# Optimization experiments

Measured on AMD Instinct MI355X. Metric: run time of the kernel, lower is better.

## Reference

```python
import jax, jax.numpy as jnp
import numpy as np

NS = (128, 128, 128)       # ns_mesh
NODES = 4                  # interpolation_nodes (P3M, even -> floor-based indexing)
N_POINTS = 100000
N_CHANNELS = 8
BOX = 10.0


def _weights_p3m4(x):
    # x: (P, 3) relative offsets in [-1/2, 1/2]; returns (4, P, 3)
    x2 = x * x
    x3 = x * x2
    c = jnp.asarray(1.0 / 48.0, dtype=x.dtype)
    return jnp.stack([
        c * (1 - 6 * x + 12 * x2 - 8 * x3),
        c * (23 - 30 * x - 12 * x2 + 24 * x3),
        c * (23 + 30 * x - 12 * x2 - 24 * x3),
        c * (1 + 6 * x + 12 * x2 + 8 * x3),
    ])


def setup_inputs() -> dict:
    key = jax.random.key(0)
    k1, k2 = jax.random.split(key)
    positions = jax.random.uniform(k1, (N_POINTS, 3), dtype=jnp.float32) * BOX
    particle_weights = jax.random.normal(k2, (N_POINTS, N_CHANNELS), dtype=jnp.float32)
    cell = jnp.eye(3, dtype=jnp.float32) * BOX
    return {"positions": positions, "particle_weights": particle_weights, "cell": cell}


def reference(positions, particle_weights, cell):
    nx, ny, nz = NS
    ns_f = jnp.array(NS, dtype=positions.dtype)
    inv_cell = jnp.linalg.inv(cell)

    # --- compute_weights ---
    pos_rel = ns_f * (positions @ inv_cell)        # (P,3) mesh-scaled fractional coords
    idx0 = jnp.floor(pos_rel)                      # even nodes -> floor of position
    offsets = pos_rel - (idx0 + 0.5)               # in [-1/2, 1/2]
    w = _weights_p3m4(offsets)                     # (4, P, 3) per-axis 1d weights
    shifts = jnp.arange(1 - (NODES + 1) // 2, 1 + NODES // 2, dtype=jnp.int32)  # [-1,0,1,2]
    ns_i = jnp.array(NS, dtype=jnp.int32)
    idx = (idx0.astype(jnp.int32)[None] + shifts[:, None, None]) % ns_i  # (4,P,3) periodic
    xi, yi, zi = idx[..., 0], idx[..., 1], idx[..., 2]  # (4,P) each

    # 3D outer product of per-axis weights: (4,4,4,P)
    w3 = w[:, None, None, :, 0] * w[None, :, None, :, 1] * w[None, None, :, :, 2]
    # flattened mesh index per (i,j,k,point): (4,4,4,P)
    lin = (xi[:, None, None] * ny + yi[None, :, None]) * nz + zi[None, None, :]

    # --- points_to_mesh: scatter-add weighted charges onto mesh ---
    C = particle_weights.shape[1]
    vals = w3[..., None] * particle_weights        # (4,4,4,P,C)
    rho_flat = jnp.zeros((nx * ny * nz, C), dtype=positions.dtype)
    rho_flat = rho_flat.at[lin.reshape(-1)].add(vals.reshape(-1, C))

    # --- mesh_to_points: gather mesh values back to particle positions ---
    gathered = rho_flat[lin]                       # (4,4,4,P,C)
    out = jnp.sum(gathered * w3[..., None], axis=(0, 1, 2))  # (P,C)
    return out
```

## Files before the change

kernel.cpp:

```cpp
#include <hip/hip_runtime.h>

static constexpr int NXC   = 128;
static constexpr int NPTS  = 100000;
static constexpr int NCH   = 8;
static constexpr int TS    = 8;
static constexpr int NT    = 16;
static constexpr int NTILES = NT * NT * NT;
static constexpr int SLOT  = 64;
static constexpr int REC   = 20;
static constexpr int SLABCAP = 32;
static constexpr int AMAX  = 14 * SLABCAP;
static constexpr int NMAX  = 48;
static constexpr int NGRP  = 32;

__device__ __forceinline__ void axis_weights(float x, float w[4]) {
    float x2 = x * x, x3 = x2 * x;
    const float c = 1.0f / 48.0f;
    w[0] = c * (1.0f  - 6.0f  * x + 12.0f * x2 - 8.0f  * x3);
    w[1] = c * (23.0f - 30.0f * x - 12.0f * x2 + 24.0f * x3);
    w[2] = c * (23.0f + 30.0f * x - 12.0f * x2 - 24.0f * x3);
    w[3] = c * (1.0f  + 6.0f  * x + 12.0f * x2 + 8.0f  * x3);
}

__device__ __forceinline__ void mesh_coords(const float* __restrict__ pos,
                                            const float* __restrict__ cell,
                                            int p, float& rx, float& ry, float& rz) {
    float a = cell[0], b = cell[1], c = cell[2];
    float d = cell[3], e = cell[4], f = cell[5];
    float g = cell[6], h = cell[7], i9 = cell[8];
    float c00 = e * i9 - f * h, c01 = f * g - d * i9, c02 = d * h - e * g;
    float c10 = c * h - b * i9, c11 = a * i9 - c * g, c12 = b * g - a * h;
    float c20 = b * f - c * e,  c21 = c * d - a * f,  c22 = a * e - b * d;
    float det = a * c00 + b * c01 + c * c02;
    float s = 128.0f / det;
    float p0 = pos[p * 3 + 0], p1 = pos[p * 3 + 1], p2 = pos[p * 3 + 2];
    rx = s * (p0 * c00 + p1 * c01 + p2 * c02);
    ry = s * (p0 * c10 + p1 * c11 + p2 * c12);
    rz = s * (p0 * c20 + p1 * c21 + p2 * c22);
}

__global__ __launch_bounds__(256) void bin_k(const float* __restrict__ pos,
                                             const float* __restrict__ pw,
                                             const float* __restrict__ cell,
                                             int* __restrict__ cursor,
                                             int* __restrict__ scell,
                                             int* __restrict__ spid,
                                             float* __restrict__ srec) {
    int p = blockIdx.x * 256 + threadIdx.x;
    if (p >= NPTS) return;
    float rx, ry, rz;
    mesh_coords(pos, cell, p, rx, ry, rz);
    float fx = floorf(rx), fy = floorf(ry), fz = floorf(rz);
    int ix = ((int)fx) & (NXC - 1), iy = ((int)fy) & (NXC - 1), iz = ((int)fz) & (NXC - 1);
    int tile = ((ix >> 3) * NT + (iy >> 3)) * NT + (iz >> 3);
    int slot = atomicAdd(cursor + tile, 1);
    if (slot >= SLOT) return;
    int idx = tile * SLOT + slot;
    scell[idx] = ix | (iy << 10) | (iz << 20);
    spid[idx] = p;
    float wx[4], wy[4], wz[4];
    axis_weights(rx - fx - 0.5f, wx);
    axis_weights(ry - fy - 0.5f, wy);
    axis_weights(rz - fz - 0.5f, wz);
    float4* r = reinterpret_cast<float4*>(srec) + (size_t)idx * 5;
    r[0] = make_float4(wx[0], wx[1], wx[2], wx[3]);
    r[1] = make_float4(wy[0], wy[1], wy[2], wy[3]);
    r[2] = make_float4(wz[0], wz[1], wz[2], wz[3]);
    const float4* pw4 = reinterpret_cast<const float4*>(pw + (size_t)p * NCH);
    r[3] = pw4[0];
    r[4] = pw4[1];
}

__device__ __forceinline__ float corr4(float4 wp, float4 wq, int d) {
    float s0 = d == 0 ? wq.x : d == -1 ? wq.y : d == -2 ? wq.z : d == -3 ? wq.w : 0.0f;
    float s1 = d == 1 ? wq.x : d ==  0 ? wq.y : d == -1 ? wq.z : d == -2 ? wq.w : 0.0f;
    float s2 = d == 2 ? wq.x : d ==  1 ? wq.y : d ==  0 ? wq.z : d == -1 ? wq.w : 0.0f;
    float s3 = d == 3 ? wq.x : d ==  2 ? wq.y : d ==  1 ? wq.z : d ==  0 ? wq.w : 0.0f;
    return wp.x * s0 + wp.y * s1 + wp.z * s2 + wp.w * s3;
}

__global__ __launch_bounds__(256) void pair_k(const int* __restrict__ cursor,
                                              const int* __restrict__ scell,
                                              const int* __restrict__ spid,
                                              const float* __restrict__ srec,
                                              float* __restrict__ out) {
    __shared__ int2 slab[AMAX];
    __shared__ int2 A12[AMAX];
    __shared__ int nlist[NGRP * NMAX];
    __shared__ int scnt[14];
    __shared__ int soff[15];

    int b = blockIdx.x;
    int tx = b >> 8, ty = (b >> 4) & 15, tz = b & 15;
    int tid = threadIdx.x;
    int lane = tid & 63;
    int nown = min(cursor[b], SLOT);
    if (nown == 0) return;
    int begin = b * SLOT;

    if (tid < 14) scnt[tid] = 0;
    __syncthreads();

    int crew = tid >> 3, cl = tid & 7;
    int base_x = tx * TS - 3, base_y = ty * TS - 3, base_z = tz * TS - 3;
    if (crew < 27) {
        int ox = crew / 9 - 1, oy = (crew / 3) % 3 - 1, oz = crew % 3 - 1;
        int nt = ((((tx + ox) & 15) * NT + ((ty + oy) & 15)) * NT) + ((tz + oz) & 15);
        int n0 = nt * SLOT;
        int cn = min(cursor[nt], SLOT);
        for (int s0 = 0; s0 < cn; s0 += 8) {
            int s = s0 + cl;
            if (s < cn) {
                int i = n0 + s;
                int c = scell[i];
                int lcx = ((c & 1023) - base_x) & 127;
                int lcy = (((c >> 10) & 1023) - base_y) & 127;
                int lcz = (((c >> 20) & 1023) - base_z) & 127;
                if (lcx < 14 && lcy < 14 && lcz < 14) {
                    int slot = atomicAdd(&scnt[lcx], 1);
                    if (slot < SLABCAP)
                        slab[lcx * SLABCAP + slot] =
                            make_int2(lcy | (lcz << 5) | (lcx << 10), i);
                }
            }
        }
    }
    __syncthreads();
    if (tid == 0) {
        int run = 0;
        #pragma unroll
        for (int s2 = 0; s2 < 14; ++s2) {
            soff[s2] = run;
            run += min(scnt[s2], SLABCAP);
        }
        soff[14] = run;
    }
    __syncthreads();
    for (int u = tid; u < AMAX; u += 256) {
        int s2 = u >> 5, i2 = u & (SLABCAP - 1);
        if (i2 < min(scnt[s2], SLABCAP)) A12[soff[s2] + i2] = slab[u];
    }
    __syncthreads();

    int sub = tid & 7, pg = tid >> 3;
    const float4* recs = reinterpret_cast<const float4*>(srec);
    int nbl = pg * NMAX;

    for (int p = pg; __any(p < nown); p += NGRP) {
        bool live = p < nown;
        int lpx = 0, lpyh = 0, lpzh = 0, jbeg = 0, span = 0, pid = 0;
        float4 pxw, pyw, pzw;
        if (live) {
            int pc = scell[begin + p];
            lpx  = (pc & 1023) - tx * TS;
            lpyh = ((pc >> 10) & 1023) - ty * TS + 3;
            lpzh = ((pc >> 20) & 1023) - tz * TS + 3;
            jbeg = soff[lpx];
            span = soff[lpx + 7] - jbeg;
            const float4* r = recs + (size_t)(begin + p) * 5;
            pxw = r[0]; pyw = r[1]; pzw = r[2];
            pid = spid[begin + p];
        }
        int creg = 0;
        for (int j0 = 0; __any(j0 < span); j0 += 8) {
            bool pass = (j0 + sub) < span;
            int a1 = 0, a2 = 0;
            if (pass) {
                int2 e = A12[jbeg + j0 + sub];
                a1 = e.x; a2 = e.y;
                int dy3 = (a1 & 31) - lpyh + 3;
                int dz3 = ((a1 >> 5) & 31) - lpzh + 3;
                pass = ((unsigned)dy3 <= 6u) && ((unsigned)dz3 <= 6u);
            }
            unsigned long long m = __ballot(pass);
            int mg = (int)(m >> (lane & 56)) & 255;
            if (pass) {
                int slot = creg + __popc(mg & ((1 << sub) - 1));
                if (slot < NMAX) {
                    int dxp3 = ((a1 >> 10) & 15) - lpx;
                    int dy3 = (a1 & 31) - lpyh + 3;
                    int dz3 = ((a1 >> 5) & 31) - lpzh + 3;
                    nlist[nbl + slot] = (a2 << 9) | (dxp3 << 6) | (dy3 << 3) | dz3;
                }
            }
            creg += __popc(mg);
        }
        int n = live ? min(creg, NMAX) : 0;
        float acc[8] = {0, 0, 0, 0, 0, 0, 0, 0};
        for (int s = sub; s < n; s += 8) {
            int ent = nlist[nbl + s];
            const float4* q = recs + (size_t)(ent >> 9) * 5;
            int dx = ((ent >> 6) & 7) - 3;
            int dy = ((ent >> 3) & 7) - 3;
            int dz = (ent & 7) - 3;
            float4 qxw = q[0], qyw = q[1], qzw = q[2];
            float S = corr4(pxw, qxw, dx) * corr4(pyw, qyw, dy) * corr4(pzw, qzw, dz);
            float4 ch0 = q[3], ch1 = q[4];
            acc[0] += S * ch0.x; acc[1] += S * ch0.y;
            acc[2] += S * ch0.z; acc[3] += S * ch0.w;
            acc[4] += S * ch1.x; acc[5] += S * ch1.y;
            acc[6] += S * ch1.z; acc[7] += S * ch1.w;
        }
        float t4[4];
        #pragma unroll
        for (int i = 0; i < 4; ++i) {
            float keep = (sub & 4) ? acc[i + 4] : acc[i];
            float send = (sub & 4) ? acc[i]     : acc[i + 4];
            t4[i] = keep + __shfl_xor(send, 4, 64);
        }
        float t2[2];
        #pragma unroll
        for (int i = 0; i < 2; ++i) {
            float keep = (sub & 2) ? t4[i + 2] : t4[i];
            float send = (sub & 2) ? t4[i]     : t4[i + 2];
            t2[i] = keep + __shfl_xor(send, 2, 64);
        }
        float keep1 = (sub & 1) ? t2[1] : t2[0];
        float send1 = (sub & 1) ? t2[0] : t2[1];
        float rres = keep1 + __shfl_xor(send1, 1, 64);
        if (live) out[(size_t)pid * NCH + sub] = rres;
    }
}

extern "C" void kernel_launch(void* const* d_in, const int* in_sizes, int n_in,
                              void* d_out, int out_size, void* d_ws, size_t ws_size,
                              hipStream_t stream) {
    const float* pos  = (const float*)d_in[0];
    const float* pw   = (const float*)d_in[1];
    const float* cell = (const float*)d_in[2];
    float* out = (float*)d_out;

    int*   cursor = (int*)d_ws;
    int*   scell  = cursor + NTILES;
    int*   spid   = scell + NTILES * SLOT;
    float* srec   = (float*)(spid + NTILES * SLOT);

    hipMemsetAsync(cursor, 0, NTILES * sizeof(int), stream);

    int pblocks = (NPTS + 255) / 256;
    bin_k<<<pblocks, 256, 0, stream>>>(pos, pw, cell, cursor, scell, spid, srec);
    pair_k<<<NTILES, 256, 0, stream>>>(cursor, scell, spid, srec, out);
}
```

Measured before the change: 61.99 us.

## Stage neighbor particle records in shared memory before pair evaluation

Before the pair loop, the block now copies the 20-float records of all candidate neighbor particles in its 14-cell halo into shared memory, capped at 224 entries. The neighbor list stores local indices rather than global particle ids, so the inner accumulation reads from LDS instead of scattered global loads. Each block pays for an up-front cooperative copy and uses about 18KB more shared memory, which may lower occupancy. The cap can also silently drop neighbors when a halo holds more than 224 candidates.

```diff
diff --git a/kernel.cpp b/kernel.cpp
--- a/kernel.cpp
+++ b/kernel.cpp
@@ -10,6 +10,7 @@
 static constexpr int REC   = 20;
 static constexpr int SLABCAP = 32;
 static constexpr int AMAX  = 14 * SLABCAP;
+static constexpr int CMAX  = 224;
 static constexpr int NMAX  = 48;
 static constexpr int NGRP  = 32;
 
@@ -85,7 +86,9 @@
                                               const float* __restrict__ srec,
                                               float* __restrict__ out) {
     __shared__ int2 slab[AMAX];
-    __shared__ int2 A12[AMAX];
+    __shared__ int A1[CMAX];
+    __shared__ int Agi[CMAX];
+    __shared__ __align__(16) float crec[CMAX * REC];
     __shared__ int nlist[NGRP * NMAX];
     __shared__ int scnt[14];
     __shared__ int soff[15];
@@ -130,20 +133,32 @@
         int run = 0;
         #pragma unroll
         for (int s2 = 0; s2 < 14; ++s2) {
-            soff[s2] = run;
+            soff[s2] = min(run, CMAX);
             run += min(scnt[s2], SLABCAP);
         }
-        soff[14] = run;
+        soff[14] = min(run, CMAX);
     }
     __syncthreads();
     for (int u = tid; u < AMAX; u += 256) {
         int s2 = u >> 5, i2 = u & (SLABCAP - 1);
-        if (i2 < min(scnt[s2], SLABCAP)) A12[soff[s2] + i2] = slab[u];
+        int cap = soff[s2 + 1] - soff[s2];
+        if (i2 < cap) {
+            int2 e = slab[u];
+            A1[soff[s2] + i2] = e.x;
+            Agi[soff[s2] + i2] = e.y;
+        }
+    }
+    __syncthreads();
+    int nc = soff[14];
+    const float4* recs = reinterpret_cast<const float4*>(srec);
+    float4* crec4 = reinterpret_cast<float4*>(crec);
+    for (int u = tid; u < nc * 5; u += 256) {
+        int j = u / 5, k = u - j * 5;
+        crec4[u] = recs[(size_t)Agi[j] * 5 + k];
     }
     __syncthreads();
 
     int sub = tid & 7, pg = tid >> 3;
-    const float4* recs = reinterpret_cast<const float4*>(srec);
     int nbl = pg * NMAX;
 
     for (int p = pg; __any(p < nown); p += NGRP) {
@@ -164,10 +179,9 @@
         int creg = 0;
         for (int j0 = 0; __any(j0 < span); j0 += 8) {
             bool pass = (j0 + sub) < span;
-            int a1 = 0, a2 = 0;
+            int a1 = 0, j = jbeg + j0 + sub;
             if (pass) {
-                int2 e = A12[jbeg + j0 + sub];
-                a1 = e.x; a2 = e.y;
+                a1 = A1[j];
                 int dy3 = (a1 & 31) - lpyh + 3;
                 int dz3 = ((a1 >> 5) & 31) - lpzh + 3;
                 pass = ((unsigned)dy3 <= 6u) && ((unsigned)dz3 <= 6u);
@@ -180,7 +194,7 @@
                     int dxp3 = ((a1 >> 10) & 15) - lpx;
                     int dy3 = (a1 & 31) - lpyh + 3;
                     int dz3 = ((a1 >> 5) & 31) - lpzh + 3;
-                    nlist[nbl + slot] = (a2 << 9) | (dxp3 << 6) | (dy3 << 3) | dz3;
+                    nlist[nbl + slot] = (j << 9) | (dxp3 << 6) | (dy3 << 3) | dz3;
                 }
             }
             creg += __popc(mg);
@@ -189,7 +203,7 @@
         float acc[8] = {0, 0, 0, 0, 0, 0, 0, 0};
         for (int s = sub; s < n; s += 8) {
             int ent = nlist[nbl + s];
-            const float4* q = recs + (size_t)(ent >> 9) * 5;
+            const float4* q = crec4 + (ent >> 9) * 5;
             int dx = ((ent >> 6) & 7) - 3;
             int dy = ((ent >> 3) & 7) - 3;
             int dz = (ent & 7) - 3;
```

Result: slower. 69.35 us (+11.9%).

## Bin particles into finer 4^3 sub-bricks and gather halo from 64 sub-bricks

Applied to the files above, without the earlier changes.

Binning now uses 32^3 sub-bricks of 4 cells with 24 slots each instead of 16^3 tiles of 64 slots. Each pair block gathers 64 neighbouring sub-bricks (4 threads each) rather than 27 tiles, and collects its owned particles from the 8 interior sub-bricks into a shared index list. The finer bins mean fewer particles outside the 14-cell halo window get scanned, which cuts wasted loads and filter work. In exchange the cursor array is 8x larger and more atomics hit it. Capacity is now 24 per sub-brick; anything beyond that overflows and is silently dropped.

```diff
diff --git a/kernel.cpp b/kernel.cpp
--- a/kernel.cpp
+++ b/kernel.cpp
@@ -6,10 +6,13 @@
 static constexpr int TS    = 8;
 static constexpr int NT    = 16;
 static constexpr int NTILES = NT * NT * NT;
-static constexpr int SLOT  = 64;
+static constexpr int NT2   = 32;
+static constexpr int NSB   = NT2 * NT2 * NT2;
+static constexpr int SLOT2 = 24;
 static constexpr int REC   = 20;
 static constexpr int SLABCAP = 32;
 static constexpr int AMAX  = 14 * SLABCAP;
+static constexpr int OMAX2 = 8 * SLOT2;
 static constexpr int NMAX  = 48;
 static constexpr int NGRP  = 32;
 
@@ -52,10 +55,10 @@
     mesh_coords(pos, cell, p, rx, ry, rz);
     float fx = floorf(rx), fy = floorf(ry), fz = floorf(rz);
     int ix = ((int)fx) & (NXC - 1), iy = ((int)fy) & (NXC - 1), iz = ((int)fz) & (NXC - 1);
-    int tile = ((ix >> 3) * NT + (iy >> 3)) * NT + (iz >> 3);
-    int slot = atomicAdd(cursor + tile, 1);
-    if (slot >= SLOT) return;
-    int idx = tile * SLOT + slot;
+    int sb = ((ix >> 2) * NT2 + (iy >> 2)) * NT2 + (iz >> 2);
+    int slot = atomicAdd(cursor + sb, 1);
+    if (slot >= SLOT2) return;
+    int idx = sb * SLOT2 + slot;
     scell[idx] = ix | (iy << 10) | (iz << 20);
     spid[idx] = p;
     float wx[4], wy[4], wz[4];
@@ -87,28 +90,38 @@
     __shared__ int2 slab[AMAX];
     __shared__ int2 A12[AMAX];
     __shared__ int nlist[NGRP * NMAX];
+    __shared__ int own[OMAX2];
     __shared__ int scnt[14];
     __shared__ int soff[15];
+    __shared__ int ocnt;
 
     int b = blockIdx.x;
     int tx = b >> 8, ty = (b >> 4) & 15, tz = b & 15;
     int tid = threadIdx.x;
     int lane = tid & 63;
-    int nown = min(cursor[b], SLOT);
-    if (nown == 0) return;
-    int begin = b * SLOT;
 
     if (tid < 14) scnt[tid] = 0;
-    __syncthreads();
-
-    int crew = tid >> 3, cl = tid & 7;
-    int base_x = tx * TS - 3, base_y = ty * TS - 3, base_z = tz * TS - 3;
-    if (crew < 27) {
-        int ox = crew / 9 - 1, oy = (crew / 3) % 3 - 1, oz = crew % 3 - 1;
-        int nt = ((((tx + ox) & 15) * NT + ((ty + oy) & 15)) * NT) + ((tz + oz) & 15);
-        int n0 = nt * SLOT;
-        int cn = min(cursor[nt], SLOT);
-        for (int s0 = 0; s0 < cn; s0 += 8) {
+    if (tid == 0) ocnt = 0;
+    __syncthreads();
+
+    {
+        int crew = tid >> 2, cl = tid & 3;
+        int ox = (crew >> 4) - 1, oy = ((crew >> 2) & 3) - 1, oz = (crew & 3) - 1;
+        int sx = (2 * tx + ox) & (NT2 - 1);
+        int sy = (2 * ty + oy) & (NT2 - 1);
+        int sz = (2 * tz + oz) & (NT2 - 1);
+        int sb = (sx * NT2 + sy) * NT2 + sz;
+        int n0 = sb * SLOT2;
+        int cn = min(cursor[sb], SLOT2);
+        bool interior = ((unsigned)ox < 2u) && ((unsigned)oy < 2u) && ((unsigned)oz < 2u);
+        int ob = 0;
+        if (interior && cl == 0 && cn > 0) ob = atomicAdd(&ocnt, cn);
+        ob = __shfl(ob, lane & 60, 64);
+        if (interior) {
+            for (int s = cl; s < cn; s += 4) own[ob + s] = n0 + s;
+        }
+        int base_x = tx * TS - 3, base_y = ty * TS - 3, base_z = tz * TS - 3;
+        for (int s0 = 0; s0 < cn; s0 += 4) {
             int s = s0 + cl;
             if (s < cn) {
                 int i = n0 + s;
@@ -126,6 +139,8 @@
         }
     }
     __syncthreads();
+    int nown = ocnt;
+    if (nown == 0) return;
     if (tid == 0) {
         int run = 0;
         #pragma unroll
@@ -151,15 +166,16 @@
         int lpx = 0, lpyh = 0, lpzh = 0, jbeg = 0, span = 0, pid = 0;
         float4 pxw, pyw, pzw;
         if (live) {
-            int pc = scell[begin + p];
+            int gi = own[p];
+            int pc = scell[gi];
             lpx  = (pc & 1023) - tx * TS;
             lpyh = ((pc >> 10) & 1023) - ty * TS + 3;
             lpzh = ((pc >> 20) & 1023) - tz * TS + 3;
             jbeg = soff[lpx];
             span = soff[lpx + 7] - jbeg;
-            const float4* r = recs + (size_t)(begin + p) * 5;
+            const float4* r = recs + (size_t)gi * 5;
             pxw = r[0]; pyw = r[1]; pzw = r[2];
-            pid = spid[begin + p];
+            pid = spid[gi];
         }
         int creg = 0;
         for (int j0 = 0; __any(j0 < span); j0 += 8) {
@@ -231,11 +247,11 @@
     float* out = (float*)d_out;
 
     int*   cursor = (int*)d_ws;
-    int*   scell  = cursor + NTILES;
-    int*   spid   = scell + NTILES * SLOT;
-    float* srec   = (float*)(spid + NTILES * SLOT);
-
-    hipMemsetAsync(cursor, 0, NTILES * sizeof(int), stream);
+    int*   scell  = cursor + NSB;
+    int*   spid   = scell + NSB * SLOT2;
+    float* srec   = (float*)(spid + NSB * SLOT2);
+
+    hipMemsetAsync(cursor, 0, NSB * sizeof(int), stream);
 
     int pblocks = (NPTS + 255) / 256;
     bin_k<<<pblocks, 256, 0, stream>>>(pos, pw, cell, cursor, scell, spid, srec);
```

Result: faster. 59.18 us, median of 2 (-4.5%).
